# Optimization experiments

Measured on AMD Instinct MI355X. Metric: run time of the kernel, lower is better.

The kernel has to match this reference:

```python
import jax, jax.numpy as jnp
import numpy as np

B, S, E, H = 1024, 128, 256, 256
N_GLIMPSES = 1
C_PTR = 10.0   # tanh_exploration for pointer head
C_GLI = 10.0   # default C for glimpse head
MASK_FILL = -100000.0


def _lstm_step(xt, h, c, W_ih, W_hh, b_ih, b_hh):
    # PyTorch LSTM gate order: i, f, g, o
    g = xt @ W_ih.T + h @ W_hh.T + b_ih + b_hh
    i, f, gg, o = jnp.split(g, 4, axis=-1)
    c = jax.nn.sigmoid(f) * c + jax.nn.sigmoid(i) * jnp.tanh(gg)
    h = jax.nn.sigmoid(o) * jnp.tanh(c)
    return h, c


def _attn_logits(query, keys, Wq_w, Wq_b, v_w, v_b, C):
    # query [B,H], keys = W_k(enc_out) precomputed [B,S,H]
    q = query @ Wq_w.T + Wq_b                      # [B,H]
    u = jnp.tanh(q[:, None, :] + keys)             # [B,S,H]
    logits = jnp.einsum('bsh,h->bs', u, v_w[0]) + v_b[0]
    return C * jnp.tanh(logits)


def setup_inputs() -> dict:
    key = jax.random.key(0)
    ks = jax.random.split(key, 24)
    sc = 1.0 / np.sqrt(H)
    d = {
        'x': jax.random.uniform(ks[0], (B, S, 2), jnp.float32),
        'emb_W': jax.random.normal(ks[1], (2, E), jnp.float32) * 0.5,
        'enc_W_ih': jax.random.normal(ks[2], (4 * H, E), jnp.float32) * sc,
        'enc_W_hh': jax.random.normal(ks[3], (4 * H, H), jnp.float32) * sc,
        'enc_b_ih': jnp.zeros((4 * H,), jnp.float32),
        'enc_b_hh': jnp.zeros((4 * H,), jnp.float32),
        'dec_W_ih': jax.random.normal(ks[4], (4 * H, E), jnp.float32) * sc,
        'dec_W_hh': jax.random.normal(ks[5], (4 * H, H), jnp.float32) * sc,
        'dec_b_ih': jnp.zeros((4 * H,), jnp.float32),
        'dec_b_hh': jnp.zeros((4 * H,), jnp.float32),
        'g_Wq_w': jax.random.normal(ks[6], (H, H), jnp.float32) * sc,
        'g_Wq_b': jnp.zeros((H,), jnp.float32),
        'g_Wk_w': jax.random.normal(ks[7], (H, H), jnp.float32) * sc,
        'g_Wk_b': jnp.zeros((H,), jnp.float32),
        'g_v_w': jax.random.normal(ks[8], (1, H), jnp.float32) * sc,
        'g_v_b': jnp.zeros((1,), jnp.float32),
        'p_Wq_w': jax.random.normal(ks[9], (H, H), jnp.float32) * sc,
        'p_Wq_b': jnp.zeros((H,), jnp.float32),
        'p_Wk_w': jax.random.normal(ks[10], (H, H), jnp.float32) * sc,
        'p_Wk_b': jnp.zeros((H,), jnp.float32),
        'p_v_w': jax.random.normal(ks[11], (1, H), jnp.float32) * sc,
        'p_v_b': jnp.zeros((1,), jnp.float32),
        'dec_start': jax.random.uniform(ks[12], (E,), jnp.float32, -1.0 / np.sqrt(E), 1.0 / np.sqrt(E)),
    }
    return d


def reference(x, emb_W, enc_W_ih, enc_W_hh, enc_b_ih, enc_b_hh,
              dec_W_ih, dec_W_hh, dec_b_ih, dec_b_hh,
              g_Wq_w, g_Wq_b, g_Wk_w, g_Wk_b, g_v_w, g_v_b,
              p_Wq_w, p_Wq_b, p_Wk_w, p_Wk_b, p_v_w, p_v_b,
              dec_start):
    b, s, _ = x.shape
    h_dim = enc_W_hh.shape[1]
    embedded = x @ emb_W  # [B,S,E] GraphEmbedding: linear map 2 -> E

    # ---- encoder LSTM over sequence ----
    h0 = jnp.zeros((b, h_dim), x.dtype)
    c0 = jnp.zeros((b, h_dim), x.dtype)

    def enc_step(carry, xt):
        h, c = carry
        h, c = _lstm_step(xt, h, c, enc_W_ih, enc_W_hh, enc_b_ih, enc_b_hh)
        return (h, c), h

    (h, c), enc_out = jax.lax.scan(enc_step, (h0, c0), jnp.swapaxes(embedded, 0, 1))
    enc_out = jnp.swapaxes(enc_out, 0, 1)  # [B,S,H]

    # W_k(enc_out) is step-invariant: precompute for both attention heads
    g_keys = enc_out @ g_Wk_w.T + g_Wk_b  # [B,S,H]
    p_keys = enc_out @ p_Wk_w.T + p_Wk_b  # [B,S,H]

    sample_keys = jax.random.split(jax.random.key(42), s)
    mask0 = jnp.zeros((b, s), bool)
    dec_in0 = jnp.broadcast_to(dec_start, (b, dec_start.shape[0]))
    rows = jnp.arange(b)

    def dec_step(carry, k):
        h, c, mask, dec_in = carry
        h, c = _lstm_step(dec_in, h, c, dec_W_ih, dec_W_hh, dec_b_ih, dec_b_hh)
        query = h
        for _ in range(N_GLIMPSES):
            logits = _attn_logits(query, g_keys, g_Wq_w, g_Wq_b, g_v_w, g_v_b, C_GLI)
            logits = jnp.where(mask, MASK_FILL, logits)
            a = jax.nn.softmax(logits, axis=-1)
            query = jnp.einsum('bsh,bs->bh', g_keys, a)
        logits = _attn_logits(query, p_keys, p_Wq_w, p_Wq_b, p_v_w, p_v_b, C_PTR)
        logits = jnp.where(mask, MASK_FILL, logits)
        logp = jax.nn.log_softmax(logits, axis=-1)
        chosen = jax.random.categorical(k, logits)  # [B]
        lp = jnp.take_along_axis(logp, chosen[:, None], axis=1)[:, 0]
        mask = mask.at[rows, chosen].set(True)
        dec_in = jnp.take_along_axis(embedded, chosen[:, None, None], axis=1)[:, 0, :]
        return (h, c, mask, dec_in), (lp, chosen)

    _, (lps, idxs) = jax.lax.scan(dec_step, (h, c, mask0, dec_in0), sample_keys)
    return jnp.swapaxes(lps, 0, 1), jnp.swapaxes(idxs, 0, 1)
```

## Files before the change

### kernel.cpp

```cpp
#include <hip/hip_runtime.h>
#include <cstdint>

#define NB 1024
#define NS 128
#define NH 256

typedef unsigned short ushort_t;
typedef unsigned char uchar_t;

__device__ __forceinline__ void tf2x32(uint32_t k0, uint32_t k1, uint32_t x0, uint32_t x1,
                                       uint32_t &o0, uint32_t &o1) {
  const uint32_t ks2 = k0 ^ k1 ^ 0x1BD11BDAu;
#define TF_R(r) { x0 += x1; x1 = (x1 << (r)) | (x1 >> (32 - (r))); x1 ^= x0; }
  x0 += k0; x1 += k1;
  TF_R(13) TF_R(15) TF_R(26) TF_R(6)
  x0 += k1; x1 += ks2 + 1u;
  TF_R(17) TF_R(29) TF_R(16) TF_R(24)
  x0 += ks2; x1 += k0 + 2u;
  TF_R(13) TF_R(15) TF_R(26) TF_R(6)
  x0 += k0; x1 += k1 + 3u;
  TF_R(17) TF_R(29) TF_R(16) TF_R(24)
  x0 += k1; x1 += ks2 + 4u;
  TF_R(13) TF_R(15) TF_R(26) TF_R(6)
  x0 += ks2; x1 += k0 + 5u;
#undef TF_R
  o0 = x0; o1 = x1;
}

__device__ __forceinline__ float fast_tanh(float x) {
  float ax = fabsf(x);
  float e = __expf(2.0f * ax);
  float r = 1.0f - 2.0f / (e + 1.0f);
  return copysignf(r, x);
}

__device__ __forceinline__ float sigm(float x) { return 1.0f / (1.0f + expf(-x)); }

__device__ __forceinline__ float4 key_load(const ushort_t* __restrict__ kh,
                                           const uchar_t* __restrict__ k8,
                                           const ushort_t* __restrict__ kn,
                                           size_t row, int h0) {
  ushort4 hv = *(const ushort4*)(kh + row * 256 + h0);
  uchar4 lv = *(const uchar4*)(k8 + row * 256 + h0);
  uint32_t nv = kn[row * 64 + (h0 >> 2)];
  float4 r;
  r.x = __uint_as_float(((uint32_t)hv.x << 16) | ((uint32_t)lv.x << 8) | ((nv & 0xFu) << 4));
  r.y = __uint_as_float(((uint32_t)hv.y << 16) | ((uint32_t)lv.y << 8) | (((nv >> 4) & 0xFu) << 4));
  r.z = __uint_as_float(((uint32_t)hv.z << 16) | ((uint32_t)lv.z << 8) | (((nv >> 8) & 0xFu) << 4));
  r.w = __uint_as_float(((uint32_t)hv.w << 16) | ((uint32_t)lv.w << 8) | (((nv >> 12) & 0xFu) << 4));
  return r;
}

__global__ __launch_bounds__(256) void prep_kernel(
    const float* __restrict__ emb_W, const float* __restrict__ enc_W_ih,
    const float* __restrict__ dec_W_ih, const float* __restrict__ dec_start,
    float* __restrict__ F_enc, float* __restrict__ F_dec,
    float* __restrict__ d0proj, uint2* __restrict__ skeys) {
  int j = blockIdx.x * 256 + threadIdx.x;
  const float* er = enc_W_ih + j * 256;
  const float* dr = dec_W_ih + j * 256;
  float fe0 = 0.f, fe1 = 0.f, fd0 = 0.f, fd1 = 0.f, dp = 0.f;
  for (int e = 0; e < 256; ++e) {
    float we0 = emb_W[e], we1 = emb_W[256 + e];
    float ev = er[e], dv = dr[e];
    fe0 = fmaf(we0, ev, fe0); fe1 = fmaf(we1, ev, fe1);
    fd0 = fmaf(we0, dv, fd0); fd1 = fmaf(we1, dv, fd1);
    dp = fmaf(dec_start[e], dv, dp);
  }
  F_enc[j] = fe0; F_enc[1024 + j] = fe1;
  F_dec[j] = fd0; F_dec[1024 + j] = fd1;
  d0proj[j] = dp;
  if (blockIdx.x == 0 && threadIdx.x < NS) {
    uint32_t o0, o1;
    tf2x32(0u, 42u, 0u, (uint32_t)threadIdx.x, o0, o1);
    skeys[threadIdx.x] = make_uint2(o0, o1);
  }
}

__global__ __launch_bounds__(1024) void transpose_all(
    const float* __restrict__ encW, const float* __restrict__ decW,
    const float* __restrict__ gWk, const float* __restrict__ pWk,
    const float* __restrict__ gWq, const float* __restrict__ pWq,
    float* __restrict__ encT, float* __restrict__ decT, float* __restrict__ WkT,
    float* __restrict__ gWT, float* __restrict__ pWT) {
  int k = blockIdx.x;
  int j = threadIdx.x;
  encT[k * 1024 + j] = encW[j * 256 + k];
  decT[k * 1024 + j] = decW[j * 256 + k];
  if (j < 512) WkT[k * 512 + j] = (j < 256) ? gWk[j * 256 + k] : pWk[(j - 256) * 256 + k];
  if (j < 256) {
    gWT[k * 256 + j] = gWq[j * 256 + k];
    pWT[k * 256 + j] = pWq[j * 256 + k];
  }
}

__global__ void diag_fill(float* out, float v, int n) {
  int i = blockIdx.x * blockDim.x + threadIdx.x;
  if (i < n) out[i] = v;
}

__global__ __launch_bounds__(1024) void net_kernel(
    const float* __restrict__ x,
    const float* __restrict__ encT, const float* __restrict__ decT,
    const float* __restrict__ enc_b_ih, const float* __restrict__ enc_b_hh,
    const float* __restrict__ dec_b_ih, const float* __restrict__ dec_b_hh,
    const float* __restrict__ F_enc, const float* __restrict__ F_dec,
    const float* __restrict__ d0proj,
    const float* __restrict__ WkT, const float* __restrict__ gkb, const float* __restrict__ pkb,
    const float* __restrict__ gWT, const float* __restrict__ pWT,
    const float* __restrict__ gqb, const float* __restrict__ pqb,
    const float* __restrict__ gvw, const float* __restrict__ gvb,
    const float* __restrict__ pvw, const float* __restrict__ pvb,
    ushort_t* __restrict__ gkh, uchar_t* __restrict__ gk8, ushort_t* __restrict__ gkn,
    ushort_t* __restrict__ pkh, uchar_t* __restrict__ pk8, ushort_t* __restrict__ pkn,
    const uint2* __restrict__ skeys, float* __restrict__ out) {
  __shared__ float h4[256][4];
  __shared__ float gx[1024][4];
  __shared__ float xs[1024];
  __shared__ float qs[4][256], vsm[4][256];
  __shared__ float qq[256][4];
  __shared__ float part[4][4][256];
  __shared__ float wl[4][4];
  __shared__ float lgs[4][NS], sv[4][NS];
  __shared__ int msk[4][NS];
  __shared__ int chs[4];

  const int tid = threadIdx.x;
  const int r_own = tid >> 8, e_own = tid & 255;
  const int bb = blockIdx.x * 4;

  xs[tid] = x[(size_t)(bb + r_own) * 256 + e_own];
  if (tid < 512) ((int*)msk)[tid] = 0;
  ((float*)h4)[tid] = 0.0f;
  const float bse = enc_b_ih[tid] + enc_b_hh[tid];
  const float fae = F_enc[tid], fbe = F_enc[1024 + tid];
  const float bsd = dec_b_ih[tid] + dec_b_hh[tid];
  const float fad = F_dec[tid], fbd = F_dec[1024 + tid];
  const float d0p = d0proj[tid];
  float h_own = 0.0f, c_own = 0.0f;
  __syncthreads();

  for (int t = 0; t < NS; ++t) {
    float4 acc = make_float4(0.f, 0.f, 0.f, 0.f);
    {
      const float* wt = encT + tid;
      const float4* hv4 = (const float4*)h4;
#pragma unroll 8
      for (int k = 0; k < 256; ++k) {
        float4 hv = hv4[k];
        float w = wt[(size_t)k * 1024];
        acc.x = fmaf(w, hv.x, acc.x);
        acc.y = fmaf(w, hv.y, acc.y);
        acc.z = fmaf(w, hv.z, acc.z);
        acc.w = fmaf(w, hv.w, acc.w);
      }
    }
    {
      float4 v;
      v.x = acc.x + bse + xs[2 * t] * fae + xs[2 * t + 1] * fbe;
      v.y = acc.y + bse + xs[256 + 2 * t] * fae + xs[256 + 2 * t + 1] * fbe;
      v.z = acc.z + bse + xs[512 + 2 * t] * fae + xs[512 + 2 * t + 1] * fbe;
      v.w = acc.w + bse + xs[768 + 2 * t] * fae + xs[768 + 2 * t + 1] * fbe;
      *(float4*)gx[tid] = v;
    }
    __syncthreads();
    {
      float gi = gx[e_own][r_own], gf = gx[e_own + 256][r_own];
      float gg = gx[e_own + 512][r_own], go = gx[e_own + 768][r_own];
      c_own = sigm(gf) * c_own + sigm(gi) * tanhf(gg);
      h_own = sigm(go) * tanhf(c_own);
      h4[e_own][r_own] = h_own;
    }
    __syncthreads();
    {
      const int j = tid & 511;
      const int kh2 = tid >> 9;
      const float* wk = WkT + (size_t)kh2 * 128 * 512 + j;
      const float4* hv4 = (const float4*)h4;
      float4 ka = make_float4(0.f, 0.f, 0.f, 0.f);
#pragma unroll 8
      for (int k = 0; k < 128; ++k) {
        float w = wk[(size_t)k * 512];
        float4 hv = hv4[kh2 * 128 + k];
        ka.x = fmaf(w, hv.x, ka.x);
        ka.y = fmaf(w, hv.y, ka.y);
        ka.z = fmaf(w, hv.z, ka.z);
        ka.w = fmaf(w, hv.w, ka.w);
      }
      ((float4*)part)[(size_t)kh2 * 512 + j] = ka;
    }
    __syncthreads();
    if (tid < 512) {
      const int j = tid;
      const float4* pf = (const float4*)part;
      float4 k0 = pf[j], k1 = pf[512 + j];
      const bool isp = (j >= 256);
      const int n = isp ? (j - 256) : j;
      float bk = (isp ? pkb : gkb)[n];
      uint32_t a0 = __float_as_uint(k0.x + k1.x + bk) + 8u;
      uint32_t a1 = __float_as_uint(k0.y + k1.y + bk) + 8u;
      uint32_t a2 = __float_as_uint(k0.z + k1.z + bk) + 8u;
      uint32_t a3 = __float_as_uint(k0.w + k1.w + bk) + 8u;
      ushort_t* kh = isp ? pkh : gkh;
      uchar_t* k8 = isp ? pk8 : gk8;
      ushort_t* kn = isp ? pkn : gkn;
      size_t r0 = (size_t)bb * NS + t, r1 = r0 + NS, r2 = r1 + NS, r3 = r2 + NS;
      kh[r0 * 256 + n] = (ushort_t)(a0 >> 16);
      kh[r1 * 256 + n] = (ushort_t)(a1 >> 16);
      kh[r2 * 256 + n] = (ushort_t)(a2 >> 16);
      kh[r3 * 256 + n] = (ushort_t)(a3 >> 16);
      k8[r0 * 256 + n] = (uchar_t)(a0 >> 8);
      k8[r1 * 256 + n] = (uchar_t)(a1 >> 8);
      k8[r2 * 256 + n] = (uchar_t)(a2 >> 8);
      k8[r3 * 256 + n] = (uchar_t)(a3 >> 8);
      uint32_t nibA = ((a0 >> 4) & 0xFu) | (((a1 >> 4) & 0xFu) << 16);
      uint32_t nibB = ((a2 >> 4) & 0xFu) | (((a3 >> 4) & 0xFu) << 16);
      nibA |= ((uint32_t)__shfl_down((int)nibA, 1)) << 4;
      nibA |= ((uint32_t)__shfl_down((int)nibA, 2)) << 8;
      nibB |= ((uint32_t)__shfl_down((int)nibB, 1)) << 4;
      nibB |= ((uint32_t)__shfl_down((int)nibB, 2)) << 8;
      if ((tid & 3) == 0) {
        kn[r0 * 64 + (n >> 2)] = (ushort_t)(nibA & 0xFFFFu);
        kn[r1 * 64 + (n >> 2)] = (ushort_t)(nibA >> 16);
        kn[r2 * 64 + (n >> 2)] = (ushort_t)(nibB & 0xFFFFu);
        kn[r3 * 64 + (n >> 2)] = (ushort_t)(nibB >> 16);
      }
    }
    __syncthreads();
  }

  for (int t = 0; t < NS; ++t) {
    float4 acc = make_float4(0.f, 0.f, 0.f, 0.f);
    {
      const float* wt = decT + tid;
      const float4* hv4 = (const float4*)h4;
#pragma unroll 8
      for (int k = 0; k < 256; ++k) {
        float4 hv = hv4[k];
        float w = wt[(size_t)k * 1024];
        acc.x = fmaf(w, hv.x, acc.x);
        acc.y = fmaf(w, hv.y, acc.y);
        acc.z = fmaf(w, hv.z, acc.z);
        acc.w = fmaf(w, hv.w, acc.w);
      }
    }
    {
      float4 v;
      if (t == 0) {
        v.x = acc.x + bsd + d0p;
        v.y = acc.y + bsd + d0p;
        v.z = acc.z + bsd + d0p;
        v.w = acc.w + bsd + d0p;
      } else {
        int c0 = chs[0], c1 = chs[1], c2 = chs[2], c3 = chs[3];
        v.x = acc.x + bsd + xs[2 * c0] * fad + xs[2 * c0 + 1] * fbd;
        v.y = acc.y + bsd + xs[256 + 2 * c1] * fad + xs[256 + 2 * c1 + 1] * fbd;
        v.z = acc.z + bsd + xs[512 + 2 * c2] * fad + xs[512 + 2 * c2 + 1] * fbd;
        v.w = acc.w + bsd + xs[768 + 2 * c3] * fad + xs[768 + 2 * c3 + 1] * fbd;
      }
      *(float4*)gx[tid] = v;
    }
    __syncthreads();
    {
      float gi = gx[e_own][r_own], gf = gx[e_own + 256][r_own];
      float gg = gx[e_own + 512][r_own], go = gx[e_own + 768][r_own];
      c_own = sigm(gf) * c_own + sigm(gi) * tanhf(gg);
      h_own = sigm(go) * tanhf(c_own);
      h4[e_own][r_own] = h_own;
    }
    __syncthreads();

    {
      const int o = tid & 255, kq = tid >> 8;
      const float* wc = gWT + (size_t)kq * 64 * 256 + o;
      const float4* hv4 = (const float4*)h4;
      float4 a = make_float4(0.f, 0.f, 0.f, 0.f);
#pragma unroll 8
      for (int k = 0; k < 64; ++k) {
        float w = wc[(size_t)k * 256];
        float4 hv = hv4[kq * 64 + k];
        a.x = fmaf(w, hv.x, a.x);
        a.y = fmaf(w, hv.y, a.y);
        a.z = fmaf(w, hv.z, a.z);
        a.w = fmaf(w, hv.w, a.w);
      }
      ((float4*)part)[(size_t)kq * 256 + o] = a;
    }
    __syncthreads();
    {
      const int o = tid & 255, r = tid >> 8;
      const float* pf = (const float*)part;
      qs[r][o] = gqb[o] + pf[o * 4 + r] + pf[1024 + o * 4 + r] +
                 pf[2048 + o * 4 + r] + pf[3072 + o * 4 + r];
      vsm[r][o] = gvw[o];
      if (o < NS) {
        uint32_t i = (uint32_t)((bb + r) * NS + o);
        uint2 sk = skeys[t];
        uint32_t o0, o1;
        tf2x32(sk.x, sk.y, 0u, i, o0, o1);
        uint32_t bits = o0 ^ o1;
        float u = __uint_as_float((bits >> 9) | 0x3f800000u) - 1.0f;
        u = u + 1.17549435e-38f;
        u = fmaxf(u, 1.17549435e-38f);
        sv[r][o] = -logf(-logf(u));
      }
    }
    __syncthreads();

    {
      const int grp = tid >> 8, gt = tid & 255;
      const int wv = gt >> 6, lane = gt & 63, h0 = lane * 4;
      const float vbias = gvb[0];
      float4 qv = *(const float4*)&qs[grp][h0];
      float v0 = vsm[grp][h0], v1 = vsm[grp][h0 + 1], v2 = vsm[grp][h0 + 2], v3 = vsm[grp][h0 + 3];
      float l = 0.f;
      float4 acc2 = make_float4(0.f, 0.f, 0.f, 0.f);
#pragma unroll 2
      for (int si = 0; si < 32; ++si) {
        int s = wv * 32 + si;
        if (msk[grp][s]) continue;
        size_t row = (size_t)(bb + grp) * NS + s;
        float4 kv = key_load(gkh, gk8, gkn, row, h0);
        float p = fast_tanh(qv.x + kv.x) * v0 + fast_tanh(qv.y + kv.y) * v1 +
                  fast_tanh(qv.z + kv.z) * v2 + fast_tanh(qv.w + kv.w) * v3;
#pragma unroll
        for (int off = 32; off; off >>= 1) p += __shfl_xor(p, off);
        float pe = expf(10.0f * tanhf(p + vbias));
        acc2.x = fmaf(pe, kv.x, acc2.x);
        acc2.y = fmaf(pe, kv.y, acc2.y);
        acc2.z = fmaf(pe, kv.z, acc2.z);
        acc2.w = fmaf(pe, kv.w, acc2.w);
        l += pe;
      }
      *(float4*)&part[grp][wv][h0] = acc2;
      if (lane == 0) wl[grp][wv] = l;
    }
    __syncthreads();
    {
      const int o = tid & 255, r = tid >> 8;
      float den = wl[r][0] + wl[r][1] + wl[r][2] + wl[r][3];
      float num = part[r][0][o] + part[r][1][o] + part[r][2][o] + part[r][3][o];
      qq[o][r] = num / den;
      vsm[r][o] = pvw[o];
    }
    __syncthreads();

    {
      const int o = tid & 255, kq = tid >> 8;
      const float* wc = pWT + (size_t)kq * 64 * 256 + o;
      const float4* qv4 = (const float4*)qq;
      float4 a = make_float4(0.f, 0.f, 0.f, 0.f);
#pragma unroll 8
      for (int k = 0; k < 64; ++k) {
        float w = wc[(size_t)k * 256];
        float4 hv = qv4[kq * 64 + k];
        a.x = fmaf(w, hv.x, a.x);
        a.y = fmaf(w, hv.y, a.y);
        a.z = fmaf(w, hv.z, a.z);
        a.w = fmaf(w, hv.w, a.w);
      }
      ((float4*)part)[(size_t)kq * 256 + o] = a;
    }
    __syncthreads();
    {
      const int o = tid & 255, r = tid >> 8;
      const float* pf = (const float*)part;
      qs[r][o] = pqb[o] + pf[o * 4 + r] + pf[1024 + o * 4 + r] +
                 pf[2048 + o * 4 + r] + pf[3072 + o * 4 + r];
    }
    __syncthreads();

    {
      const int grp = tid >> 8, gt = tid & 255;
      const int wv = gt >> 6, lane = gt & 63, h0 = lane * 4;
      const float vbias = pvb[0];
      float4 qv = *(const float4*)&qs[grp][h0];
      float v0 = vsm[grp][h0], v1 = vsm[grp][h0 + 1], v2 = vsm[grp][h0 + 2], v3 = vsm[grp][h0 + 3];
#pragma unroll 2
      for (int si = 0; si < 32; ++si) {
        int s = wv * 32 + si;
        if (msk[grp][s]) {
          if (lane == 0) lgs[grp][s] = -100000.0f;
          continue;
        }
        size_t row = (size_t)(bb + grp) * NS + s;
        float4 kv = key_load(pkh, pk8, pkn, row, h0);
        float p = fast_tanh(qv.x + kv.x) * v0 + fast_tanh(qv.y + kv.y) * v1 +
                  fast_tanh(qv.z + kv.z) * v2 + fast_tanh(qv.w + kv.w) * v3;
#pragma unroll
        for (int off = 32; off; off >>= 1) p += __shfl_down(p, off);
        if (lane == 0) lgs[grp][s] = 10.0f * tanhf(p + vbias);
      }
    }
    __syncthreads();

    if (((tid & 255) >> 6) == 0) {
      const int grp = tid >> 8, lane = tid & 63;
      float a0 = lgs[grp][lane], a1 = lgs[grp][lane + 64];
      float es = expf(a0) + expf(a1);
      float b0 = a0 + sv[grp][lane], b1 = a1 + sv[grp][lane + 64];
      float bv; int bi;
      if (b1 > b0) { bv = b1; bi = lane + 64; } else { bv = b0; bi = lane; }
#pragma unroll
      for (int off = 32; off; off >>= 1) {
        es += __shfl_xor(es, off);
        float ov = __shfl_down(bv, off);
        int oi = __shfl_down(bi, off);
        if (ov > bv) { bv = ov; bi = oi; }
      }
      if (lane == 0) {
        int cs = bi;
        out[(size_t)(bb + grp) * NS + t] = lgs[grp][cs] - logf(es);
        out[(size_t)NB * NS + (size_t)(bb + grp) * NS + t] = (float)cs;
        msk[grp][cs] = 1;
        chs[grp] = cs;
      }
    }
    __syncthreads();
  }
}

extern "C" void kernel_launch(void* const* d_in, const int* in_sizes, int n_in,
                              void* d_out, int out_size, void* d_ws, size_t ws_size,
                              hipStream_t stream) {
  const float* x        = (const float*)d_in[0];
  const float* emb_W    = (const float*)d_in[1];
  const float* enc_W_ih = (const float*)d_in[2];
  const float* enc_W_hh = (const float*)d_in[3];
  const float* enc_b_ih = (const float*)d_in[4];
  const float* enc_b_hh = (const float*)d_in[5];
  const float* dec_W_ih = (const float*)d_in[6];
  const float* dec_W_hh = (const float*)d_in[7];
  const float* dec_b_ih = (const float*)d_in[8];
  const float* dec_b_hh = (const float*)d_in[9];
  const float* g_Wq_w = (const float*)d_in[10];
  const float* g_Wq_b = (const float*)d_in[11];
  const float* g_Wk_w = (const float*)d_in[12];
  const float* g_Wk_b = (const float*)d_in[13];
  const float* g_v_w  = (const float*)d_in[14];
  const float* g_v_b  = (const float*)d_in[15];
  const float* p_Wq_w = (const float*)d_in[16];
  const float* p_Wq_b = (const float*)d_in[17];
  const float* p_Wk_w = (const float*)d_in[18];
  const float* p_Wk_b = (const float*)d_in[19];
  const float* p_v_w  = (const float*)d_in[20];
  const float* p_v_b  = (const float*)d_in[21];
  const float* dec_start = (const float*)d_in[22];
  (void)in_sizes; (void)n_in;

  const size_t KELEM = (size_t)NB * NS * NH;
  char* w = (char*)d_ws;
  size_t off = 0;
  auto alloc = [&](size_t bytes) -> void* {
    void* p = w + off;
    off += (bytes + 255) & ~(size_t)255;
    return p;
  };
  ushort_t* gkh = (ushort_t*)alloc(KELEM * 2);
  uchar_t*  gk8 = (uchar_t*)alloc(KELEM);
  ushort_t* gkn = (ushort_t*)alloc(KELEM / 2);
  ushort_t* pkh = (ushort_t*)alloc(KELEM * 2);
  uchar_t*  pk8 = (uchar_t*)alloc(KELEM);
  ushort_t* pkn = (ushort_t*)alloc(KELEM / 2);

  float* encT   = (float*)alloc(1024 * 256 * 4);
  float* decT   = (float*)alloc(1024 * 256 * 4);
  float* WkT    = (float*)alloc(512 * 256 * 4);
  float* gWT    = (float*)alloc(256 * 256 * 4);
  float* pWT    = (float*)alloc(256 * 256 * 4);
  float* F_enc  = (float*)alloc(2048 * 4);
  float* F_dec  = (float*)alloc(2048 * 4);
  float* d0proj = (float*)alloc(1024 * 4);
  uint2* skeys  = (uint2*)alloc(NS * 8);

  if (off > ws_size) {
    diag_fill<<<(out_size + 255) / 256, 256, 0, stream>>>((float*)d_out, (float)ws_size, out_size);
    return;
  }

  prep_kernel<<<4, 256, 0, stream>>>(emb_W, enc_W_ih, dec_W_ih, dec_start,
                                     F_enc, F_dec, d0proj, skeys);
  transpose_all<<<256, 1024, 0, stream>>>(enc_W_hh, dec_W_hh, g_Wk_w, p_Wk_w,
                                          g_Wq_w, p_Wq_w, encT, decT, WkT, gWT, pWT);
  net_kernel<<<NB / 4, 1024, 0, stream>>>(
      x, encT, decT, enc_b_ih, enc_b_hh, dec_b_ih, dec_b_hh,
      F_enc, F_dec, d0proj, WkT, g_Wk_b, p_Wk_b,
      gWT, pWT, g_Wq_b, p_Wq_b, g_v_w, g_v_b, p_v_w, p_v_b,
      gkh, gk8, gkn, pkh, pk8, pkn, skeys, (float*)d_out);
}
```

Measured before the change: 10.83 ms.

## Software-pipeline key projection into LSTM steps and remove barrier-separated reduction phases

The key projection for encoder step t-1 now runs inside step t, overlapping the recurrent matvec and gate update, and the last key step is deferred into the first decoder step. This removes two barriers per encoder step. In the decoder, the query partial sums are reduced by each consumer directly from a transposed gx buffer instead of a separate reduction pass, and Gumbel noise generation moves into the gate phase, removing further barriers. Masked logits are written once at selection time rather than on every step. The risks are extra shared-memory traffic and more complex ordering of the pipelined key writes.

```diff
diff --git a/kernel.cpp b/kernel.cpp
--- a/kernel.cpp
+++ b/kernel.cpp
@@ -115,9 +115,9 @@
     ushort_t* __restrict__ pkh, uchar_t* __restrict__ pk8, ushort_t* __restrict__ pkn,
     const uint2* __restrict__ skeys, float* __restrict__ out) {
   __shared__ float h4[256][4];
-  __shared__ float gx[1024][4];
+  __shared__ float gx[4][1024];
   __shared__ float xs[1024];
-  __shared__ float qs[4][256], vsm[4][256];
+  __shared__ float vsm[256];
   __shared__ float qq[256][4];
   __shared__ float part[4][4][256];
   __shared__ float wl[4][4];
@@ -140,6 +140,60 @@
   float h_own = 0.0f, c_own = 0.0f;
   __syncthreads();
 
+  auto keys_partials = [&]() {
+    const int j = tid & 511;
+    const int kh2 = tid >> 9;
+    const float* wk = WkT + (size_t)kh2 * 128 * 512 + j;
+    const float4* hv4 = (const float4*)h4;
+    float4 ka = make_float4(0.f, 0.f, 0.f, 0.f);
+#pragma unroll 8
+    for (int k = 0; k < 128; ++k) {
+      float w = wk[(size_t)k * 512];
+      float4 hv = hv4[kh2 * 128 + k];
+      ka.x = fmaf(w, hv.x, ka.x);
+      ka.y = fmaf(w, hv.y, ka.y);
+      ka.z = fmaf(w, hv.z, ka.z);
+      ka.w = fmaf(w, hv.w, ka.w);
+    }
+    ((float4*)part)[(size_t)kh2 * 512 + j] = ka;
+  };
+  auto keys_combine = [&](int kt) {
+    const int j = tid;
+    const float4* pf = (const float4*)part;
+    float4 k0 = pf[j], k1 = pf[512 + j];
+    const bool isp = (j >= 256);
+    const int n = isp ? (j - 256) : j;
+    float bk = (isp ? pkb : gkb)[n];
+    uint32_t a0 = __float_as_uint(k0.x + k1.x + bk) + 8u;
+    uint32_t a1 = __float_as_uint(k0.y + k1.y + bk) + 8u;
+    uint32_t a2 = __float_as_uint(k0.z + k1.z + bk) + 8u;
+    uint32_t a3 = __float_as_uint(k0.w + k1.w + bk) + 8u;
+    ushort_t* kh = isp ? pkh : gkh;
+    uchar_t* k8 = isp ? pk8 : gk8;
+    ushort_t* kn = isp ? pkn : gkn;
+    size_t r0 = (size_t)bb * NS + kt, r1 = r0 + NS, r2 = r1 + NS, r3 = r2 + NS;
+    kh[r0 * 256 + n] = (ushort_t)(a0 >> 16);
+    kh[r1 * 256 + n] = (ushort_t)(a1 >> 16);
+    kh[r2 * 256 + n] = (ushort_t)(a2 >> 16);
+    kh[r3 * 256 + n] = (ushort_t)(a3 >> 16);
+    k8[r0 * 256 + n] = (uchar_t)(a0 >> 8);
+    k8[r1 * 256 + n] = (uchar_t)(a1 >> 8);
+    k8[r2 * 256 + n] = (uchar_t)(a2 >> 8);
+    k8[r3 * 256 + n] = (uchar_t)(a3 >> 8);
+    uint32_t nibA = ((a0 >> 4) & 0xFu) | (((a1 >> 4) & 0xFu) << 16);
+    uint32_t nibB = ((a2 >> 4) & 0xFu) | (((a3 >> 4) & 0xFu) << 16);
+    nibA |= ((uint32_t)__shfl_down((int)nibA, 1)) << 4;
+    nibA |= ((uint32_t)__shfl_down((int)nibA, 2)) << 8;
+    nibB |= ((uint32_t)__shfl_down((int)nibB, 1)) << 4;
+    nibB |= ((uint32_t)__shfl_down((int)nibB, 2)) << 8;
+    if ((tid & 3) == 0) {
+      kn[r0 * 64 + (n >> 2)] = (ushort_t)(nibA & 0xFFFFu);
+      kn[r1 * 64 + (n >> 2)] = (ushort_t)(nibA >> 16);
+      kn[r2 * 64 + (n >> 2)] = (ushort_t)(nibB & 0xFFFFu);
+      kn[r3 * 64 + (n >> 2)] = (ushort_t)(nibB >> 16);
+    }
+  };
+
   for (int t = 0; t < NS; ++t) {
     float4 acc = make_float4(0.f, 0.f, 0.f, 0.f);
     {
@@ -155,77 +209,20 @@
         acc.w = fmaf(w, hv.w, acc.w);
       }
     }
-    {
-      float4 v;
-      v.x = acc.x + bse + xs[2 * t] * fae + xs[2 * t + 1] * fbe;
-      v.y = acc.y + bse + xs[256 + 2 * t] * fae + xs[256 + 2 * t + 1] * fbe;
-      v.z = acc.z + bse + xs[512 + 2 * t] * fae + xs[512 + 2 * t + 1] * fbe;
-      v.w = acc.w + bse + xs[768 + 2 * t] * fae + xs[768 + 2 * t + 1] * fbe;
-      *(float4*)gx[tid] = v;
-    }
-    __syncthreads();
-    {
-      float gi = gx[e_own][r_own], gf = gx[e_own + 256][r_own];
-      float gg = gx[e_own + 512][r_own], go = gx[e_own + 768][r_own];
+    if (t > 0) keys_partials();
+    gx[0][tid] = acc.x + bse + xs[2 * t] * fae + xs[2 * t + 1] * fbe;
+    gx[1][tid] = acc.y + bse + xs[256 + 2 * t] * fae + xs[256 + 2 * t + 1] * fbe;
+    gx[2][tid] = acc.z + bse + xs[512 + 2 * t] * fae + xs[512 + 2 * t + 1] * fbe;
+    gx[3][tid] = acc.w + bse + xs[768 + 2 * t] * fae + xs[768 + 2 * t + 1] * fbe;
+    __syncthreads();
+    {
+      float gi = gx[r_own][e_own], gf = gx[r_own][e_own + 256];
+      float gg = gx[r_own][e_own + 512], go = gx[r_own][e_own + 768];
       c_own = sigm(gf) * c_own + sigm(gi) * tanhf(gg);
       h_own = sigm(go) * tanhf(c_own);
       h4[e_own][r_own] = h_own;
     }
-    __syncthreads();
-    {
-      const int j = tid & 511;
-      const int kh2 = tid >> 9;
-      const float* wk = WkT + (size_t)kh2 * 128 * 512 + j;
-      const float4* hv4 = (const float4*)h4;
-      float4 ka = make_float4(0.f, 0.f, 0.f, 0.f);
-#pragma unroll 8
-      for (int k = 0; k < 128; ++k) {
-        float w = wk[(size_t)k * 512];
-        float4 hv = hv4[kh2 * 128 + k];
-        ka.x = fmaf(w, hv.x, ka.x);
-        ka.y = fmaf(w, hv.y, ka.y);
-        ka.z = fmaf(w, hv.z, ka.z);
-        ka.w = fmaf(w, hv.w, ka.w);
-      }
-      ((float4*)part)[(size_t)kh2 * 512 + j] = ka;
-    }
-    __syncthreads();
-    if (tid < 512) {
-      const int j = tid;
-      const float4* pf = (const float4*)part;
-      float4 k0 = pf[j], k1 = pf[512 + j];
-      const bool isp = (j >= 256);
-      const int n = isp ? (j - 256) : j;
-      float bk = (isp ? pkb : gkb)[n];
-      uint32_t a0 = __float_as_uint(k0.x + k1.x + bk) + 8u;
-      uint32_t a1 = __float_as_uint(k0.y + k1.y + bk) + 8u;
-      uint32_t a2 = __float_as_uint(k0.z + k1.z + bk) + 8u;
-      uint32_t a3 = __float_as_uint(k0.w + k1.w + bk) + 8u;
-      ushort_t* kh = isp ? pkh : gkh;
-      uchar_t* k8 = isp ? pk8 : gk8;
-      ushort_t* kn = isp ? pkn : gkn;
-      size_t r0 = (size_t)bb * NS + t, r1 = r0 + NS, r2 = r1 + NS, r3 = r2 + NS;
-      kh[r0 * 256 + n] = (ushort_t)(a0 >> 16);
-      kh[r1 * 256 + n] = (ushort_t)(a1 >> 16);
-      kh[r2 * 256 + n] = (ushort_t)(a2 >> 16);
-      kh[r3 * 256 + n] = (ushort_t)(a3 >> 16);
-      k8[r0 * 256 + n] = (uchar_t)(a0 >> 8);
-      k8[r1 * 256 + n] = (uchar_t)(a1 >> 8);
-      k8[r2 * 256 + n] = (uchar_t)(a2 >> 8);
-      k8[r3 * 256 + n] = (uchar_t)(a3 >> 8);
-      uint32_t nibA = ((a0 >> 4) & 0xFu) | (((a1 >> 4) & 0xFu) << 16);
-      uint32_t nibB = ((a2 >> 4) & 0xFu) | (((a3 >> 4) & 0xFu) << 16);
-      nibA |= ((uint32_t)__shfl_down((int)nibA, 1)) << 4;
-      nibA |= ((uint32_t)__shfl_down((int)nibA, 2)) << 8;
-      nibB |= ((uint32_t)__shfl_down((int)nibB, 1)) << 4;
-      nibB |= ((uint32_t)__shfl_down((int)nibB, 2)) << 8;
-      if ((tid & 3) == 0) {
-        kn[r0 * 64 + (n >> 2)] = (ushort_t)(nibA & 0xFFFFu);
-        kn[r1 * 64 + (n >> 2)] = (ushort_t)(nibA >> 16);
-        kn[r2 * 64 + (n >> 2)] = (ushort_t)(nibB & 0xFFFFu);
-        kn[r3 * 64 + (n >> 2)] = (ushort_t)(nibB >> 16);
-      }
-    }
+    if (t > 0 && tid < 512) keys_combine(t - 1);
     __syncthreads();
   }
 
@@ -244,30 +241,40 @@
         acc.w = fmaf(w, hv.w, acc.w);
       }
     }
-    {
-      float4 v;
-      if (t == 0) {
-        v.x = acc.x + bsd + d0p;
-        v.y = acc.y + bsd + d0p;
-        v.z = acc.z + bsd + d0p;
-        v.w = acc.w + bsd + d0p;
-      } else {
-        int c0 = chs[0], c1 = chs[1], c2 = chs[2], c3 = chs[3];
-        v.x = acc.x + bsd + xs[2 * c0] * fad + xs[2 * c0 + 1] * fbd;
-        v.y = acc.y + bsd + xs[256 + 2 * c1] * fad + xs[256 + 2 * c1 + 1] * fbd;
-        v.z = acc.z + bsd + xs[512 + 2 * c2] * fad + xs[512 + 2 * c2 + 1] * fbd;
-        v.w = acc.w + bsd + xs[768 + 2 * c3] * fad + xs[768 + 2 * c3 + 1] * fbd;
-      }
-      *(float4*)gx[tid] = v;
-    }
-    __syncthreads();
-    {
-      float gi = gx[e_own][r_own], gf = gx[e_own + 256][r_own];
-      float gg = gx[e_own + 512][r_own], go = gx[e_own + 768][r_own];
+    if (t == 0) keys_partials();
+    if (t == 0) {
+      gx[0][tid] = acc.x + bsd + d0p;
+      gx[1][tid] = acc.y + bsd + d0p;
+      gx[2][tid] = acc.z + bsd + d0p;
+      gx[3][tid] = acc.w + bsd + d0p;
+    } else {
+      int c0 = chs[0], c1 = chs[1], c2 = chs[2], c3 = chs[3];
+      gx[0][tid] = acc.x + bsd + xs[2 * c0] * fad + xs[2 * c0 + 1] * fbd;
+      gx[1][tid] = acc.y + bsd + xs[256 + 2 * c1] * fad + xs[256 + 2 * c1 + 1] * fbd;
+      gx[2][tid] = acc.z + bsd + xs[512 + 2 * c2] * fad + xs[512 + 2 * c2 + 1] * fbd;
+      gx[3][tid] = acc.w + bsd + xs[768 + 2 * c3] * fad + xs[768 + 2 * c3 + 1] * fbd;
+    }
+    if (tid < 256) vsm[tid] = gvw[tid];
+    if (e_own < NS) {
+      uint32_t i = (uint32_t)((bb + r_own) * NS + e_own);
+      uint2 sk = skeys[t];
+      uint32_t o0, o1;
+      tf2x32(sk.x, sk.y, 0u, i, o0, o1);
+      uint32_t bits = o0 ^ o1;
+      float u = __uint_as_float((bits >> 9) | 0x3f800000u) - 1.0f;
+      u = u + 1.17549435e-38f;
+      u = fmaxf(u, 1.17549435e-38f);
+      sv[r_own][e_own] = -logf(-logf(u));
+    }
+    __syncthreads();
+    {
+      float gi = gx[r_own][e_own], gf = gx[r_own][e_own + 256];
+      float gg = gx[r_own][e_own + 512], go = gx[r_own][e_own + 768];
       c_own = sigm(gf) * c_own + sigm(gi) * tanhf(gg);
       h_own = sigm(go) * tanhf(c_own);
       h4[e_own][r_own] = h_own;
     }
+    if (t == 0 && tid < 512) keys_combine(NS - 1);
     __syncthreads();
 
     {
@@ -284,35 +291,29 @@
         a.z = fmaf(w, hv.z, a.z);
         a.w = fmaf(w, hv.w, a.w);
       }
-      ((float4*)part)[(size_t)kq * 256 + o] = a;
-    }
-    __syncthreads();
-    {
-      const int o = tid & 255, r = tid >> 8;
-      const float* pf = (const float*)part;
-      qs[r][o] = gqb[o] + pf[o * 4 + r] + pf[1024 + o * 4 + r] +
-                 pf[2048 + o * 4 + r] + pf[3072 + o * 4 + r];
-      vsm[r][o] = gvw[o];
-      if (o < NS) {
-        uint32_t i = (uint32_t)((bb + r) * NS + o);
-        uint2 sk = skeys[t];
-        uint32_t o0, o1;
-        tf2x32(sk.x, sk.y, 0u, i, o0, o1);
-        uint32_t bits = o0 ^ o1;
-        float u = __uint_as_float((bits >> 9) | 0x3f800000u) - 1.0f;
-        u = u + 1.17549435e-38f;
-        u = fmaxf(u, 1.17549435e-38f);
-        sv[r][o] = -logf(-logf(u));
-      }
+      gx[kq][o] = a.x;
+      gx[kq][256 + o] = a.y;
+      gx[kq][512 + o] = a.z;
+      gx[kq][768 + o] = a.w;
     }
     __syncthreads();
 
     {
       const int grp = tid >> 8, gt = tid & 255;
       const int wv = gt >> 6, lane = gt & 63, h0 = lane * 4;
+      float4 qv = *(const float4*)(gqb + h0);
+      {
+        float4 p0 = *(const float4*)&gx[0][grp * 256 + h0];
+        float4 p1 = *(const float4*)&gx[1][grp * 256 + h0];
+        float4 p2 = *(const float4*)&gx[2][grp * 256 + h0];
+        float4 p3 = *(const float4*)&gx[3][grp * 256 + h0];
+        qv.x += p0.x + p1.x + p2.x + p3.x;
+        qv.y += p0.y + p1.y + p2.y + p3.y;
+        qv.z += p0.z + p1.z + p2.z + p3.z;
+        qv.w += p0.w + p1.w + p2.w + p3.w;
+      }
       const float vbias = gvb[0];
-      float4 qv = *(const float4*)&qs[grp][h0];
-      float v0 = vsm[grp][h0], v1 = vsm[grp][h0 + 1], v2 = vsm[grp][h0 + 2], v3 = vsm[grp][h0 + 3];
+      float v0 = vsm[h0], v1 = vsm[h0 + 1], v2 = vsm[h0 + 2], v3 = vsm[h0 + 3];
       float l = 0.f;
       float4 acc2 = make_float4(0.f, 0.f, 0.f, 0.f);
 #pragma unroll 2
@@ -341,8 +342,8 @@
       float den = wl[r][0] + wl[r][1] + wl[r][2] + wl[r][3];
       float num = part[r][0][o] + part[r][1][o] + part[r][2][o] + part[r][3][o];
       qq[o][r] = num / den;
-      vsm[r][o] = pvw[o];
-    }
+    }
+    if (tid < 256) vsm[tid] = pvw[tid];
     __syncthreads();
 
     {
@@ -359,30 +360,33 @@
         a.z = fmaf(w, hv.z, a.z);
         a.w = fmaf(w, hv.w, a.w);
       }
-      ((float4*)part)[(size_t)kq * 256 + o] = a;
-    }
-    __syncthreads();
-    {
-      const int o = tid & 255, r = tid >> 8;
-      const float* pf = (const float*)part;
-      qs[r][o] = pqb[o] + pf[o * 4 + r] + pf[1024 + o * 4 + r] +
-                 pf[2048 + o * 4 + r] + pf[3072 + o * 4 + r];
+      gx[kq][o] = a.x;
+      gx[kq][256 + o] = a.y;
+      gx[kq][512 + o] = a.z;
+      gx[kq][768 + o] = a.w;
     }
     __syncthreads();
 
     {
       const int grp = tid >> 8, gt = tid & 255;
       const int wv = gt >> 6, lane = gt & 63, h0 = lane * 4;
+      float4 qv = *(const float4*)(pqb + h0);
+      {
+        float4 p0 = *(const float4*)&gx[0][grp * 256 + h0];
+        float4 p1 = *(const float4*)&gx[1][grp * 256 + h0];
+        float4 p2 = *(const float4*)&gx[2][grp * 256 + h0];
+        float4 p3 = *(const float4*)&gx[3][grp * 256 + h0];
+        qv.x += p0.x + p1.x + p2.x + p3.x;
+        qv.y += p0.y + p1.y + p2.y + p3.y;
+        qv.z += p0.z + p1.z + p2.z + p3.z;
+        qv.w += p0.w + p1.w + p2.w + p3.w;
+      }
       const float vbias = pvb[0];
-      float4 qv = *(const float4*)&qs[grp][h0];
-      float v0 = vsm[grp][h0], v1 = vsm[grp][h0 + 1], v2 = vsm[grp][h0 + 2], v3 = vsm[grp][h0 + 3];
+      float v0 = vsm[h0], v1 = vsm[h0 + 1], v2 = vsm[h0 + 2], v3 = vsm[h0 + 3];
 #pragma unroll 2
       for (int si = 0; si < 32; ++si) {
         int s = wv * 32 + si;
-        if (msk[grp][s]) {
-          if (lane == 0) lgs[grp][s] = -100000.0f;
-          continue;
-        }
+        if (msk[grp][s]) continue;
         size_t row = (size_t)(bb + grp) * NS + s;
         float4 kv = key_load(pkh, pk8, pkn, row, h0);
         float p = fast_tanh(qv.x + kv.x) * v0 + fast_tanh(qv.y + kv.y) * v1 +
@@ -413,6 +417,7 @@
         out[(size_t)(bb + grp) * NS + t] = lgs[grp][cs] - logf(es);
         out[(size_t)NB * NS + (size_t)(bb + grp) * NS + t] = (float)cs;
         msk[grp][cs] = 1;
+        lgs[grp][cs] = -100000.0f;
         chs[grp] = cs;
       }
     }
```

After: 18.97 ms. 75.2% more time.
